# Optimization experiments

Measured on AMD Instinct MI355X. Metric: run time of the kernel, lower is better.

Reference implementation:

```python
import jax, jax.numpy as jnp
import numpy as np

B, N, F_IN, F_OUT = 1024, 16, 1024, 4096  # n_nodes=16 and n_heads=1 are structurally fixed by the module


def setup_inputs() -> dict:
    key = jax.random.key(0)
    ks = jax.random.split(key, 7)
    s1 = 1.0 / np.sqrt(F_IN)
    s2 = 1.0 / np.sqrt(F_IN * 16)
    return {
        "x": jax.random.normal(ks[0], (B, N, F_IN), jnp.float32),
        "matrix": jax.random.uniform(ks[1], (B, N, N), jnp.float32),
        "W1": jax.random.uniform(ks[2], (F_IN, F_IN), jnp.float32, -s1, s1),
        "b1": jax.random.uniform(ks[3], (F_IN,), jnp.float32, -s1, s1),
        "W_mlp": jax.random.uniform(ks[4], (F_OUT, F_IN * 16), jnp.float32, -s2, s2),
        "b_mlp": jax.random.uniform(ks[5], (F_OUT,), jnp.float32, -s2, s2),
        "a_param": jnp.float32(5.0),
    }


def _l2norm(v):
    # matches F.normalize(p=2, dim=-1, eps=1e-12)
    n = jnp.maximum(jnp.linalg.norm(v, axis=-1, keepdims=True), 1e-12)
    return v / n


def _forward(x, matrix, W1, b1, W_mlp, b_mlp, a_param):
    Bc, n, f = x.shape  # n_heads = 1, n_hidden = f
    wg = x @ W1.T + b1                                    # [B,n,f]
    gs = _l2norm(x)                                       # g_reshaped (H=1)
    gt = _l2norm(wg)                                      # g_transposed
    e = jnp.einsum('bik,bjk->bij', gs, gt)[..., None]     # [B,n,n,1] cosine scores
    eye = jnp.eye(n, dtype=x.dtype)[None, :, :, None]
    e = e * (1.0 + eye * a_param)                         # boost diagonal
    a_scores = e                                          # pre-softmax scores (used below)
    esm = jax.nn.softmax(e, axis=1)                       # softmax over dim=1
    m = matrix[..., None]                                 # [B,n,n,1]
    # MPUGAT message passing
    from_i = jnp.einsum('bitp,btkp->bikp', esm, m)        # [B,n,n,1]
    diag = jnp.einsum('bkkp->bkp', m)                     # diagonal of matrix
    from_j = esm * diag[:, None, :, :]                    # '...jkp,...kkp->...jkp'
    e2 = jnp.einsum('bikp,bjkp->bijp', from_i, from_j)    # [B,n,n,1]
    e2 = 0.5 * (e2 + jnp.transpose(e2, (0, 2, 1, 3)))
    # attention readout with PRE-softmax scores a_scores
    g = x.reshape(Bc, n, 1, f)                            # [B,n,H=1,f]
    attn = jnp.tanh(jnp.einsum('bjhf,bjih->bihf', g, a_scores))  # [B,n,1,f]
    out = attn.reshape(Bc, -1) @ W_mlp.T + b_mlp          # [B,F_OUT]
    out = jnp.broadcast_to(out[:, None, :], (Bc, 16, out.shape[-1]))  # repeat(1,16,1)
    return out, e2, m


def reference(x, matrix, W1, b1, W_mlp, b_mlp, a_param):
    return _forward(x, matrix, W1, b1, W_mlp, b_mlp, a_param)
```

## Files before the change

### kernel.cpp

```cpp
#include <hip/hip_runtime.h>
#include <math.h>

typedef short short8 __attribute__((ext_vector_type(8)));
typedef float f32x4 __attribute__((ext_vector_type(4)));
typedef unsigned short us4 __attribute__((ext_vector_type(4)));
typedef unsigned int u32x4 __attribute__((ext_vector_type(4)));
typedef unsigned short u16;
typedef unsigned int u32;

#define GAS __attribute__((address_space(1)))
#define LAS __attribute__((address_space(3)))

static __device__ __forceinline__ u16 f2bf(float f) {
    union { float f; u32 u; } v; v.f = f;
    u32 r = v.u + 0x7FFFu + ((v.u >> 16) & 1u);
    return (u16)(r >> 16);
}

static __device__ __forceinline__ u32 pk2(float a, float b) {
    return (u32)f2bf(a) | ((u32)f2bf(b) << 16);
}

static __device__ __forceinline__ u32 cvtpk(float lo, float hi) {
    u32 r;
    asm("v_cvt_pk_bf16_f32 %0, %1, %2" : "=v"(r) : "v"(lo), "v"(hi));
    return r;
}

static __device__ __forceinline__ float bf2f(u16 h) {
    union { u32 u; float f; } v; v.u = ((u32)h) << 16;
    return v.f;
}

static __device__ __forceinline__ void gll16(const void* g, void* l) {
    __builtin_amdgcn_global_load_lds((const GAS void*)g, (LAS void*)l, 16, 0, 0);
}

__global__ __launch_bounds__(256) void k_cvt_x(const float* __restrict__ x,
                                               u16* __restrict__ xb,
                                               float* __restrict__ xinv) {
    const int row = blockIdx.x, t = threadIdx.x;
    const f32x4 v = *(const f32x4*)(x + (size_t)row * 1024 + 4 * t);
    u32* dst = (u32*)(xb + (size_t)row * 1024 + 4 * t);
    dst[0] = pk2(v.x, v.y); dst[1] = pk2(v.z, v.w);
    float s = v.x * v.x + v.y * v.y + v.z * v.z + v.w * v.w;
#pragma unroll
    for (int off = 1; off < 64; off <<= 1) s += __shfl_xor(s, off, 64);
    __shared__ float red[4];
    if ((t & 63) == 0) red[t >> 6] = s;
    __syncthreads();
    if (t == 0)
        xinv[row] = 1.0f / fmaxf(sqrtf(red[0] + red[1] + red[2] + red[3]), 1e-12f);
}

__global__ __launch_bounds__(256) void k_cvt(const float* __restrict__ in,
                                             u16* __restrict__ out) {
    const size_t i = (size_t)blockIdx.x * 256 + threadIdx.x;
    const f32x4 v = *(const f32x4*)(in + 4 * i);
    u32* dst = (u32*)(out + 4 * i);
    dst[0] = pk2(v.x, v.y); dst[1] = pk2(v.z, v.w);
}

#define MFMA16(a, b, c) __builtin_amdgcn_mfma_f32_16x16x32_bf16(a, b, c, 0, 0, 0)
#define SBAR() __builtin_amdgcn_s_barrier()
#define LGKM0() do { asm volatile("s_waitcnt lgkmcnt(0)" ::: "memory"); __builtin_amdgcn_sched_barrier(0); } while (0)
#define SCHED0() __builtin_amdgcn_sched_barrier(0)
#define VMW4 asm volatile("s_waitcnt vmcnt(4)" ::: "memory")
#define VMW2 asm volatile("s_waitcnt vmcnt(2)" ::: "memory")
#define VMW0 asm volatile("s_waitcnt vmcnt(0)" ::: "memory")
#define VMW8L asm volatile("s_waitcnt vmcnt(8) lgkmcnt(0)" ::: "memory")
#define VMW0L asm volatile("s_waitcnt vmcnt(0) lgkmcnt(0)" ::: "memory")
#define LGKML asm volatile("s_waitcnt lgkmcnt(0)" ::: "memory")
#define VMNOP do {} while (0)

#define DO_TILE(ISS, VMA, VMB, VMD)                                           \
  do {                                                                        \
    short8 Af[4][2], Bf0[2][2], Bf1[2][2];                                    \
    _Pragma("unroll") for (int m = 0; m < 4; ++m) {                           \
      Af[m][0] = *(const short8*)(la + rpA[m] + sw0);                         \
      Af[m][1] = *(const short8*)(la + rpA[m] + sw1);                         \
    }                                                                         \
    _Pragma("unroll") for (int n = 0; n < 2; ++n) {                           \
      Bf0[n][0] = *(const short8*)(lb + rpB[n] + sw0);                        \
      Bf0[n][1] = *(const short8*)(lb + rpB[n] + sw1);                        \
    }                                                                         \
    if (ISS) { gll16(AG + (saO00 + knx), danext + ldst);                      \
               gll16(AG + (saO01 + knx), danext + 4096 + ldst); }             \
    SBAR(); LGKM0();                                                          \
    __builtin_amdgcn_s_setprio(1);                                            \
    _Pragma("unroll") for (int m = 0; m < 4; ++m)                             \
      _Pragma("unroll") for (int n = 0; n < 2; ++n) {                         \
        acc[m][n] = MFMA16(Af[m][0], Bf0[n][0], acc[m][n]);                   \
        acc[m][n] = MFMA16(Af[m][1], Bf0[n][1], acc[m][n]);                   \
      }                                                                       \
    __builtin_amdgcn_s_setprio(0); SCHED0(); VMA; SBAR();                     \
    _Pragma("unroll") for (int n = 0; n < 2; ++n) {                           \
      Bf1[n][0] = *(const short8*)(lb + rpB[n + 2] + sw0);                    \
      Bf1[n][1] = *(const short8*)(lb + rpB[n + 2] + sw1);                    \
    }                                                                         \
    if (ISS) { gll16(BG + (sbO00 + knx), dbnext + ldst);                      \
               gll16(BG + (sbO01 + knx), dbnext + 4096 + ldst); }             \
    SBAR(); LGKM0();                                                          \
    __builtin_amdgcn_s_setprio(1);                                            \
    _Pragma("unroll") for (int m = 0; m < 4; ++m)                             \
      _Pragma("unroll") for (int n = 0; n < 2; ++n) {                         \
        acc[m][n + 2] = MFMA16(Af[m][0], Bf1[n][0], acc[m][n + 2]);           \
        acc[m][n + 2] = MFMA16(Af[m][1], Bf1[n][1], acc[m][n + 2]);           \
      }                                                                       \
    __builtin_amdgcn_s_setprio(0); SCHED0(); VMB; SBAR();                     \
    _Pragma("unroll") for (int m = 0; m < 4; ++m) {                           \
      Af[m][0] = *(const short8*)(la + rpA[m + 4] + sw0);                     \
      Af[m][1] = *(const short8*)(la + rpA[m + 4] + sw1);                     \
    }                                                                         \
    if (ISS) { gll16(BG + (sbO10 + knx), dbnext + 8192 + ldst);               \
               gll16(BG + (sbO11 + knx), dbnext + 8192 + 4096 + ldst); }      \
    SBAR(); LGKM0();                                                          \
    __builtin_amdgcn_s_setprio(1);                                            \
    _Pragma("unroll") for (int m = 0; m < 4; ++m)                             \
      _Pragma("unroll") for (int n = 0; n < 2; ++n) {                         \
        acc[m + 4][n] = MFMA16(Af[m][0], Bf0[n][0], acc[m + 4][n]);           \
        acc[m + 4][n] = MFMA16(Af[m][1], Bf0[n][1], acc[m + 4][n]);           \
      }                                                                       \
    __builtin_amdgcn_s_setprio(0); SCHED0(); SBAR();                          \
    if (ISS) { gll16(AG + (saO10 + knx), danext + 8192 + ldst);               \
               gll16(AG + (saO11 + knx), danext + 8192 + 4096 + ldst); }      \
    __builtin_amdgcn_s_setprio(1);                                            \
    _Pragma("unroll") for (int m = 0; m < 4; ++m)                             \
      _Pragma("unroll") for (int n = 0; n < 2; ++n) {                         \
        acc[m + 4][n + 2] = MFMA16(Af[m][1], Bf1[n][1], acc[m + 4][n + 2]);   \
        acc[m + 4][n + 2] = MFMA16(Af[m][0], Bf1[n][0], acc[m + 4][n + 2]);   \
      }                                                                       \
    __builtin_amdgcn_s_setprio(0); SCHED0(); VMD; SBAR();                     \
  } while (0)

#define GT2S(ISS, KNXA, KNXB, WAITX)                                          \
  do {                                                                        \
    short8 Af[4][2], Bf0[2][2], Bf1[2][2];                                    \
    _Pragma("unroll") for (int m = 0; m < 4; ++m) {                           \
      Af[m][0] = *(const short8*)(la + rpA[m] + sw0);                         \
      Af[m][1] = *(const short8*)(la + rpA[m] + sw1);                         \
    }                                                                         \
    _Pragma("unroll") for (int n = 0; n < 2; ++n) {                           \
      Bf0[n][0] = *(const short8*)(lb + rpB[n] + sw0);                        \
      Bf0[n][1] = *(const short8*)(lb + rpB[n] + sw1);                        \
    }                                                                         \
    if (ISS) { gll16(AG + (saO00 + (KNXA)), danext + ldst);                   \
               gll16(AG + (saO01 + (KNXA)), danext + 4096 + ldst); }          \
    SBAR(); LGKM0();                                                          \
    __builtin_amdgcn_s_setprio(1);                                            \
    _Pragma("unroll") for (int k = 0; k < 2; ++k)                             \
      _Pragma("unroll") for (int m = 0; m < 4; ++m)                           \
        _Pragma("unroll") for (int n = 0; n < 2; ++n)                         \
          acc[m][n] = MFMA16(Af[m][k], Bf0[n][k], acc[m][n]);                 \
    __builtin_amdgcn_s_setprio(0); SCHED0(); SBAR();                          \
    _Pragma("unroll") for (int n = 0; n < 2; ++n) {                           \
      Bf1[n][0] = *(const short8*)(lb + rpB[n + 2] + sw0);                    \
      Bf1[n][1] = *(const short8*)(lb + rpB[n + 2] + sw1);                    \
    }                                                                         \
    if (ISS) { gll16(AG + (saO10 + (KNXA)), danext + 8192 + ldst);            \
               gll16(AG + (saO11 + (KNXA)), danext + 8192 + 4096 + ldst); }   \
    SBAR(); LGKM0();                                                          \
    __builtin_amdgcn_s_setprio(1);                                            \
    _Pragma("unroll") for (int k = 0; k < 2; ++k)                             \
      _Pragma("unroll") for (int m = 0; m < 4; ++m)                           \
        _Pragma("unroll") for (int n = 0; n < 2; ++n)                         \
          acc[m][n + 2] = MFMA16(Af[m][k], Bf1[n][k], acc[m][n + 2]);         \
    __builtin_amdgcn_s_setprio(0); SCHED0(); SBAR();                          \
    _Pragma("unroll") for (int m = 0; m < 4; ++m) {                           \
      Af[m][0] = *(const short8*)(la + rpA[m + 4] + sw0);                     \
      Af[m][1] = *(const short8*)(la + rpA[m + 4] + sw1);                     \
    }                                                                         \
    SBAR(); LGKM0();                                                          \
    __builtin_amdgcn_s_setprio(1);                                            \
    _Pragma("unroll") for (int k = 0; k < 2; ++k)                             \
      _Pragma("unroll") for (int m = 0; m < 4; ++m)                           \
        _Pragma("unroll") for (int n = 0; n < 2; ++n)                         \
          acc[m + 4][n] = MFMA16(Af[m][k], Bf0[n][k], acc[m + 4][n]);         \
    __builtin_amdgcn_s_setprio(0); SCHED0();                                  \
    if (ISS) {                                                                \
      _Pragma("unroll") for (int c = 0; c < 2; ++c) {                         \
        u32x4 wv;                                                             \
        wv.x = cvtpk(bn[2 * c].x, bn[2 * c].y);                               \
        wv.y = cvtpk(bn[2 * c].z, bn[2 * c].w);                               \
        wv.z = cvtpk(bn[2 * c + 1].x, bn[2 * c + 1].y);                       \
        wv.w = cvtpk(bn[2 * c + 1].z, bn[2 * c + 1].w);                       \
        *(u32x4*)(dbnext + c * 4096 + (tid << 3)) = wv;                       \
        bn[2 * c]     = *(const f32x4*)(BGf + bro[c] + (KNXB) + swsrc);       \
        bn[2 * c + 1] = *(const f32x4*)(BGf + bro[c] + (KNXB) + swsrc + 4);   \
      }                                                                       \
    }                                                                         \
    SBAR();                                                                   \
    __builtin_amdgcn_s_setprio(1);                                            \
    _Pragma("unroll") for (int k = 0; k < 2; ++k)                             \
      _Pragma("unroll") for (int m = 0; m < 4; ++m)                           \
        _Pragma("unroll") for (int n = 0; n < 2; ++n)                         \
          acc[m + 4][n + 2] = MFMA16(Af[m][k], Bf1[n][k], acc[m + 4][n + 2]); \
    __builtin_amdgcn_s_setprio(0); SCHED0();                                  \
    if (ISS) {                                                                \
      _Pragma("unroll") for (int c = 2; c < 4; ++c) {                         \
        u32x4 wv;                                                             \
        wv.x = cvtpk(bn[2 * c].x, bn[2 * c].y);                               \
        wv.y = cvtpk(bn[2 * c].z, bn[2 * c].w);                               \
        wv.z = cvtpk(bn[2 * c + 1].x, bn[2 * c + 1].y);                       \
        wv.w = cvtpk(bn[2 * c + 1].z, bn[2 * c + 1].w);                       \
        *(u32x4*)(dbnext + c * 4096 + (tid << 3)) = wv;                       \
        bn[2 * c]     = *(const f32x4*)(BGf + bro[c] + (KNXB) + swsrc);       \
        bn[2 * c + 1] = *(const f32x4*)(BGf + bro[c] + (KNXB) + swsrc + 4);   \
      }                                                                       \
    }                                                                         \
    WAITX; SBAR();                                                            \
  } while (0)

__global__ __launch_bounds__(512, 2) void k_gemm1_8ph(const u16* __restrict__ AG,
                                                      const u16* __restrict__ BG,
                                                      const float* __restrict__ bias,
                                                      u16* __restrict__ C,
                                                      float* __restrict__ wgn2) {
    __shared__ __align__(16) u16 LsA[2][16384];
    __shared__ __align__(16) u16 LsB[2][16384];
    const int K = 1024, NT = 16;
    const int lin = blockIdx.x;
    const int w = (lin & 7) * 32 + (lin >> 3);
    const int n0 = (w & 3) * 256;
    const int m0 = (w >> 2) * 256;

    const int tid = threadIdx.x, wave = tid >> 6, lane = tid & 63;
    const int lr = lane & 15, kq = lane >> 4;
    const int wr = wave >> 2, wc = wave & 3;

    const int trow = tid >> 3;
    const u32 swsrc = (u32)(((tid & 7) ^ (trow & 7)) * 8);
    const u32 saO00 = (u32)(m0 + 0 + trow) * (u32)K + swsrc;
    const u32 saO01 = (u32)(m0 + 128 + trow) * (u32)K + swsrc;
    const u32 saO10 = (u32)(m0 + 64 + trow) * (u32)K + swsrc;
    const u32 saO11 = (u32)(m0 + 192 + trow) * (u32)K + swsrc;
    const int q0 = trow, q1 = 64 + trow;
    const u32 sbO00 = (u32)(n0 + (q0 >> 5) * 64 + (q0 & 31)) * (u32)K + swsrc;
    const u32 sbO01 = (u32)(n0 + (q1 >> 5) * 64 + (q1 & 31)) * (u32)K + swsrc;
    const u32 sbO10 = (u32)(n0 + (q0 >> 5) * 64 + 32 + (q0 & 31)) * (u32)K + swsrc;
    const u32 sbO11 = (u32)(n0 + (q1 >> 5) * 64 + 32 + (q1 & 31)) * (u32)K + swsrc;
    const u32 ldst = (u32)wave * 512;

    int rpA[8], rpB[4];
#pragma unroll
    for (int mf = 0; mf < 8; ++mf)
        rpA[mf] = ((mf >> 2) * 128 + wr * 64 + (mf & 3) * 16 + lr) << 6;
#pragma unroll
    for (int nf = 0; nf < 4; ++nf)
        rpB[nf] = ((nf >> 1) * 128 + wc * 32 + (nf & 1) * 16 + lr) << 6;
    const int sw0 = ((0 + kq) ^ (lr & 7)) * 8;
    const int sw1 = ((4 + kq) ^ (lr & 7)) * 8;

    f32x4 acc[8][4] = {};

    gll16(AG + saO00, &LsA[0][0] + ldst);
    gll16(AG + saO01, &LsA[0][0] + 4096 + ldst);
    gll16(BG + sbO00, &LsB[0][0] + ldst);
    gll16(BG + sbO01, &LsB[0][0] + 4096 + ldst);
    gll16(BG + sbO10, &LsB[0][0] + 8192 + ldst);
    gll16(BG + sbO11, &LsB[0][0] + 8192 + 4096 + ldst);
    gll16(AG + saO10, &LsA[0][0] + 8192 + ldst);
    gll16(AG + saO11, &LsA[0][0] + 8192 + 4096 + ldst);
    VMW4;
    SBAR();

    int cur = 0;
    u32 ko = 64;
    for (int T = 0; T < NT - 1; ++T) {
        const u16* la = &LsA[cur][0];
        const u16* lb = &LsB[cur][0];
        u16* danext = &LsA[cur ^ 1][0];
        u16* dbnext = &LsB[cur ^ 1][0];
        const u32 knx = ko;
        DO_TILE(1, VMW4, VMW4, VMW4);
        cur ^= 1;
        ko += 64;
    }
    {
        const u16* la = &LsA[cur][0];
        const u16* lb = &LsB[cur][0];
        u16* danext = &LsA[cur ^ 1][0];
        u16* dbnext = &LsB[cur ^ 1][0];
        const u32 knx = 0;
        (void)danext; (void)dbnext;
        DO_TILE(0, VMW2, VMW0, VMNOP);
    }

    const int col0 = n0 + wc * 64;
    const int row0 = m0 + wr * 128;
    float bcol[4];
#pragma unroll
    for (int nf = 0; nf < 4; ++nf) bcol[nf] = bias[col0 + nf * 16 + lr];
#pragma unroll
    for (int mf = 0; mf < 8; ++mf) {
#pragma unroll
        for (int r = 0; r < 4; ++r) {
            const int row = row0 + mf * 16 + kq * 4 + r;
            float nrm = 0.f;
#pragma unroll
            for (int nf = 0; nf < 4; ++nf) {
                float v = acc[mf][nf][r] + bcol[nf];
                C[(size_t)row * 1024 + col0 + nf * 16 + lr] = f2bf(v);
                nrm += v * v;
            }
#pragma unroll
            for (int off = 1; off < 16; off <<= 1) nrm += __shfl_xor(nrm, off, 64);
            if (lr == 0) atomicAdd(&wgn2[row], nrm);
        }
    }
}

__global__ __launch_bounds__(512, 2) void k_gemm2_8ph(const u16* __restrict__ AG,
                                                      const float* __restrict__ BGf,
                                                      u16* __restrict__ part) {
    __shared__ __align__(16) u16 LsA[2][16384];
    __shared__ __align__(16) u16 LsB[2][16384];
    const int K = 16384, NT = 64;
    const int lin = blockIdx.x;
    const int w = (lin & 7) * 32 + (lin >> 3);
    const int m0 = (w & 3) * 256;
    const int z = (w >> 2) & 3;
    const int n0 = (w >> 4) * 256;
    const int kbeg = z * 4096;

    const int tid = threadIdx.x, wave = tid >> 6, lane = tid & 63;
    const int lr = lane & 15, kq = lane >> 4;
    const int wr = wave >> 2, wc = wave & 3;

    const int trow = tid >> 3;
    const u32 swsrc = (u32)(((tid & 7) ^ (trow & 7)) * 8);
    const u32 saO00 = (u32)(m0 + 0 + trow) * (u32)K + (u32)kbeg + swsrc;
    const u32 saO01 = (u32)(m0 + 128 + trow) * (u32)K + (u32)kbeg + swsrc;
    const u32 saO10 = (u32)(m0 + 64 + trow) * (u32)K + (u32)kbeg + swsrc;
    const u32 saO11 = (u32)(m0 + 192 + trow) * (u32)K + (u32)kbeg + swsrc;
    const int q0 = trow, q1 = 64 + trow;
    u32 bro[4];
    bro[0] = (u32)(n0 + (q0 >> 5) * 64 + (q0 & 31)) * 16384u + (u32)kbeg;
    bro[1] = (u32)(n0 + (q1 >> 5) * 64 + (q1 & 31)) * 16384u + (u32)kbeg;
    bro[2] = bro[0] + 32u * 16384u;
    bro[3] = bro[1] + 32u * 16384u;
    const u32 ldst = (u32)wave * 512;

    int rpA[8], rpB[4];
#pragma unroll
    for (int mf = 0; mf < 8; ++mf)
        rpA[mf] = ((mf >> 2) * 128 + wr * 64 + (mf & 3) * 16 + lr) << 6;
#pragma unroll
    for (int nf = 0; nf < 4; ++nf)
        rpB[nf] = ((nf >> 1) * 128 + wc * 32 + (nf & 1) * 16 + lr) << 6;
    const int sw0 = ((0 + kq) ^ (lr & 7)) * 8;
    const int sw1 = ((4 + kq) ^ (lr & 7)) * 8;

    f32x4 acc[8][4] = {};
    f32x4 bn[8];

    {
#pragma unroll
        for (int c = 0; c < 4; ++c) {
            bn[2 * c]     = *(const f32x4*)(BGf + bro[c] + swsrc);
            bn[2 * c + 1] = *(const f32x4*)(BGf + bro[c] + swsrc + 4);
        }
        gll16(AG + saO00, &LsA[0][0] + ldst);
        gll16(AG + saO01, &LsA[0][0] + 4096 + ldst);
        gll16(AG + saO10, &LsA[0][0] + 8192 + ldst);
        gll16(AG + saO11, &LsA[0][0] + 8192 + 4096 + ldst);
#pragma unroll
        for (int c = 0; c < 4; ++c) {
            u32x4 wv;
            wv.x = cvtpk(bn[2 * c].x, bn[2 * c].y);
            wv.y = cvtpk(bn[2 * c].z, bn[2 * c].w);
            wv.z = cvtpk(bn[2 * c + 1].x, bn[2 * c + 1].y);
            wv.w = cvtpk(bn[2 * c + 1].z, bn[2 * c + 1].w);
            *(u32x4*)(&LsB[0][0] + c * 4096 + (tid << 3)) = wv;
        }
        asm volatile("s_waitcnt vmcnt(0) lgkmcnt(0)" ::: "memory");
#pragma unroll
        for (int c = 0; c < 4; ++c) {
            bn[2 * c]     = *(const f32x4*)(BGf + bro[c] + 64 + swsrc);
            bn[2 * c + 1] = *(const f32x4*)(BGf + bro[c] + 64 + swsrc + 4);
        }
        SBAR();
    }

    int cur = 0;
    for (int T = 0; T < NT - 1; ++T) {
        const u16* la = &LsA[cur][0];
        const u16* lb = &LsB[cur][0];
        u16* danext = &LsA[cur ^ 1][0];
        u16* dbnext = &LsB[cur ^ 1][0];
        const u32 knxa = (u32)(T + 1) * 64;
        const u32 knxb = (T + 2 < NT) ? (u32)(T + 2) * 64 : 0u;
        GT2S(1, knxa, knxb, VMW8L);
        cur ^= 1;
    }
    {
        const u16* la = &LsA[cur][0];
        const u16* lb = &LsB[cur][0];
        u16* danext = &LsA[cur ^ 1][0];
        u16* dbnext = &LsB[cur ^ 1][0];
        (void)danext; (void)dbnext;
        GT2S(0, 0u, 0u, LGKML);
    }

    u16* po = part + (size_t)z * 4194304ull;
    const int col0 = n0 + wc * 64;
    const int row0 = m0 + wr * 128;
#pragma unroll
    for (int mf = 0; mf < 8; ++mf)
#pragma unroll
        for (int r = 0; r < 4; ++r) {
            const int row = row0 + mf * 16 + kq * 4 + r;
#pragma unroll
            for (int nf = 0; nf < 4; ++nf)
                po[(size_t)row * 4096 + col0 + nf * 16 + lr] = f2bf(acc[mf][nf][r]);
        }
}

__global__ __launch_bounds__(256) void k_batch_attn(const u16* xb,
                                                    const u16* __restrict__ wgb,
                                                    const float* __restrict__ xinv,
                                                    const float* __restrict__ wgn2,
                                                    const float* __restrict__ matrix,
                                                    const float* __restrict__ a_param,
                                                    float* __restrict__ e2_out,
                                                    float* __restrict__ m_out,
                                                    u16* attn_bf) {
    const int b = blockIdx.x, tid = threadIdx.x;
    const int wave = tid >> 6, lane = tid & 63;
    const int j = lane & 15, ig = (lane >> 4) * 4;

    __shared__ float qred[4][64][4];
    __shared__ float esm_l[16 * 17];
    __shared__ float fi_l[16 * 17];
    __shared__ float e2_l[16 * 17];
    __shared__ float m_l[256];
    __shared__ float as_l[256];
    __shared__ float xsh[16][256];

    {
        const size_t roff = (size_t)(b * 16 + j) * 1024 + (lane >> 4) * 8 + wave * 256;
        f32x4 acc0 = {}, acc1 = {};
#pragma unroll
        for (int kt = 0; kt < 256; kt += 64) {
            short8 xa0 = *(const short8*)(xb + roff + kt);
            short8 wa0 = *(const short8*)(wgb + roff + kt);
            short8 xa1 = *(const short8*)(xb + roff + kt + 32);
            short8 wa1 = *(const short8*)(wgb + roff + kt + 32);
            acc0 = __builtin_amdgcn_mfma_f32_16x16x32_bf16(xa0, wa0, acc0, 0, 0, 0);
            acc1 = __builtin_amdgcn_mfma_f32_16x16x32_bf16(xa1, wa1, acc1, 0, 0, 0);
        }
#pragma unroll
        for (int r = 0; r < 4; ++r) qred[wave][lane][r] = acc0[r] + acc1[r];
    }
    __syncthreads();

    if (tid < 64) {
        const int l = tid;
        const float inw = 1.0f / fmaxf(sqrtf(wgn2[b * 16 + j]), 1e-12f);
        const float boost = 1.0f + a_param[0];
        float e[4];
#pragma unroll
        for (int r = 0; r < 4; ++r) {
            const int i = ig + r;
            float v = (qred[0][l][r] + qred[1][l][r] + qred[2][l][r] + qred[3][l][r]) *
                      xinv[b * 16 + i] * inw;
            if (i == j) v *= boost;
            e[r] = v;
            as_l[i * 16 + j] = v;
        }
        float mx = fmaxf(fmaxf(e[0], e[1]), fmaxf(e[2], e[3]));
        mx = fmaxf(mx, __shfl_xor(mx, 16, 64));
        mx = fmaxf(mx, __shfl_xor(mx, 32, 64));
        float p[4], s = 0.f;
#pragma unroll
        for (int r = 0; r < 4; ++r) { p[r] = __expf(e[r] - mx); s += p[r]; }
        s += __shfl_xor(s, 16, 64);
        s += __shfl_xor(s, 32, 64);
        const float invs = 1.0f / s;
#pragma unroll
        for (int r = 0; r < 4; ++r) esm_l[(ig + r) * 17 + j] = p[r] * invs;
        const f32x4 mv = *(const f32x4*)(matrix + (size_t)b * 256 + 4 * l);
        *(f32x4*)(m_l + 4 * l) = mv;
        *(f32x4*)(m_out + (size_t)b * 256 + 4 * l) = mv;
    }
    __syncthreads();
    if (tid < 64) {
        float fi[4] = {0, 0, 0, 0};
#pragma unroll
        for (int t = 0; t < 16; ++t) {
            const float mk = m_l[t * 16 + j];
#pragma unroll
            for (int r = 0; r < 4; ++r) fi[r] += esm_l[(ig + r) * 17 + t] * mk;
        }
#pragma unroll
        for (int r = 0; r < 4; ++r) fi_l[(ig + r) * 17 + j] = fi[r];
    }
    __syncthreads();
    if (tid < 64) {
        float e2v[4] = {0, 0, 0, 0};
#pragma unroll
        for (int kk = 0; kk < 16; ++kk) {
            const float wgt = esm_l[j * 17 + kk] * m_l[kk * 16 + kk];
#pragma unroll
            for (int r = 0; r < 4; ++r) e2v[r] += fi_l[(ig + r) * 17 + kk] * wgt;
        }
#pragma unroll
        for (int r = 0; r < 4; ++r) e2_l[(ig + r) * 17 + j] = e2v[r];
    }
    __syncthreads();
    if (tid < 64) {
#pragma unroll
        for (int r = 0; r < 4; ++r) {
            const int i = ig + r;
            e2_out[(size_t)b * 256 + i * 16 + j] =
                0.5f * (e2_l[i * 17 + j] + e2_l[j * 17 + i]);
        }
    }

    for (int ch = 0; ch < 4; ++ch) {
        __syncthreads();
#pragma unroll
        for (int jj = 0; jj < 16; ++jj)
            xsh[jj][tid] = bf2f(xb[((size_t)b * 16 + jj) * 1024 + ch * 256 + tid]);
        __syncthreads();
        float accv[16] = {};
#pragma unroll
        for (int jj = 0; jj < 16; ++jj) {
            const float xv = xsh[jj][tid];
#pragma unroll
            for (int i = 0; i < 16; ++i) accv[i] = fmaf(as_l[jj * 16 + i], xv, accv[i]);
        }
#pragma unroll
        for (int i = 0; i < 16; ++i)
            attn_bf[((size_t)b * 16 + i) * 1024 + ch * 256 + tid] = f2bf(tanhf(accv[i]));
    }
}

__global__ __launch_bounds__(256) void k_bcast(const u16* __restrict__ p,
                                               const float* __restrict__ bias,
                                               float* __restrict__ out) {
    const size_t i = (size_t)blockIdx.x * 256 + threadIdx.x;
    const int o4 = (int)(i & 1023);
    const int b = (int)(i >> 14);
    const size_t src = (size_t)b * 4096 + (size_t)o4 * 4;
    f32x4 r = *(const f32x4*)(bias + (size_t)o4 * 4);
#pragma unroll
    for (int z = 0; z < 4; ++z) {
        us4 v = *(const us4*)(p + (size_t)z * 4194304ull + src);
        r.x += bf2f(v.x); r.y += bf2f(v.y); r.z += bf2f(v.z); r.w += bf2f(v.w);
    }
    *(f32x4*)(out + i * 4) = r;
}

extern "C" void kernel_launch(void* const* d_in, const int* in_sizes, int n_in,
                              void* d_out, int out_size, void* d_ws, size_t ws_size,
                              hipStream_t stream) {
    const float* x      = (const float*)d_in[0];
    const float* matrix = (const float*)d_in[1];
    const float* W1     = (const float*)d_in[2];
    const float* b1     = (const float*)d_in[3];
    const float* W_mlp  = (const float*)d_in[4];
    const float* b_mlp  = (const float*)d_in[5];
    const float* a_par  = (const float*)d_in[6];
    float* out = (float*)d_out;

    char* ws = (char*)d_ws;
    size_t off = 0;
    auto alloc = [&](size_t bytes) {
        char* p = ws + off;
        off += (bytes + 255) & ~(size_t)255;
        return p;
    };
    u16*   x_bf  = (u16*)alloc(16384ull * 1024 * 2);
    u16*   wg_bf = (u16*)alloc(16384ull * 1024 * 2);
    u16*   w1_bf = (u16*)alloc(1024ull * 1024 * 2);
    float* xinv  = (float*)alloc(16384ull * 4);
    float* wgn2  = (float*)alloc(16384ull * 4);
    u16*   attn_bf = x_bf;
    u16*   part    = wg_bf;
    float* e2_out = out + 67108864ull;
    float* m_out  = out + 67371008ull;

    hipMemsetAsync(wgn2, 0, 16384 * 4, stream);
    k_cvt_x<<<16384, 256, 0, stream>>>(x, x_bf, xinv);
    k_cvt<<<1024, 256, 0, stream>>>(W1, w1_bf);
    k_gemm1_8ph<<<256, 512, 0, stream>>>(x_bf, w1_bf, b1, wg_bf, wgn2);
    k_batch_attn<<<1024, 256, 0, stream>>>(x_bf, wg_bf, xinv, wgn2, matrix, a_par,
                                           e2_out, m_out, attn_bf);
    k_gemm2_8ph<<<256, 512, 0, stream>>>(attn_bf, W_mlp, part);
    k_bcast<<<65536, 256, 0, stream>>>(part, b_mlp, out);
}
```

Before: 370.1 us.

## Fuse W1 conversion into x conversion, reorder MFMAs, vectorize staging, fast tanh

Folds the W1 bf16 conversion into the x conversion kernel through extra blocks, removing one launch. Reorders the MFMA loops in the GEMM tile macro to iterate k outermost and drops two barriers. In the attention kernel, x is now staged in LDS as bf16 using 16-byte vector loads instead of scalar loads converted to float. tanhf is replaced with an exp-based formula. The barrier removal risks races, and the fast tanh changes rounding slightly.

Measured after the change: 339.3 us. 8.3% less time.

```diff
diff --git a/kernel.cpp b/kernel.cpp
--- a/kernel.cpp
+++ b/kernel.cpp
@@ -32,14 +32,30 @@
     return v.f;
 }
 
+static __device__ __forceinline__ float ftanh(float v) {
+    float t = __expf(-2.0f * fabsf(v));
+    float r = (1.0f - t) / (1.0f + t);
+    return copysignf(r, v);
+}
+
 static __device__ __forceinline__ void gll16(const void* g, void* l) {
     __builtin_amdgcn_global_load_lds((const GAS void*)g, (LAS void*)l, 16, 0, 0);
 }
 
 __global__ __launch_bounds__(256) void k_cvt_x(const float* __restrict__ x,
                                                u16* __restrict__ xb,
-                                               float* __restrict__ xinv) {
-    const int row = blockIdx.x, t = threadIdx.x;
+                                               float* __restrict__ xinv,
+                                               const float* __restrict__ W1,
+                                               u16* __restrict__ w1b) {
+    const int bid = blockIdx.x, t = threadIdx.x;
+    if (bid >= 16384) {
+        const size_t i = (size_t)(bid - 16384) * 256 + t;
+        const f32x4 v = *(const f32x4*)(W1 + 4 * i);
+        u32* dst = (u32*)(w1b + 4 * i);
+        dst[0] = pk2(v.x, v.y); dst[1] = pk2(v.z, v.w);
+        return;
+    }
+    const int row = bid;
     const f32x4 v = *(const f32x4*)(x + (size_t)row * 1024 + 4 * t);
     u32* dst = (u32*)(xb + (size_t)row * 1024 + 4 * t);
     dst[0] = pk2(v.x, v.y); dst[1] = pk2(v.z, v.w);
@@ -51,14 +67,6 @@
     __syncthreads();
     if (t == 0)
         xinv[row] = 1.0f / fmaxf(sqrtf(red[0] + red[1] + red[2] + red[3]), 1e-12f);
-}
-
-__global__ __launch_bounds__(256) void k_cvt(const float* __restrict__ in,
-                                             u16* __restrict__ out) {
-    const size_t i = (size_t)blockIdx.x * 256 + threadIdx.x;
-    const f32x4 v = *(const f32x4*)(in + 4 * i);
-    u32* dst = (u32*)(out + 4 * i);
-    dst[0] = pk2(v.x, v.y); dst[1] = pk2(v.z, v.w);
 }
 
 #define MFMA16(a, b, c) __builtin_amdgcn_mfma_f32_16x16x32_bf16(a, b, c, 0, 0, 0)
@@ -69,7 +77,6 @@
 #define VMW2 asm volatile("s_waitcnt vmcnt(2)" ::: "memory")
 #define VMW0 asm volatile("s_waitcnt vmcnt(0)" ::: "memory")
 #define VMW8L asm volatile("s_waitcnt vmcnt(8) lgkmcnt(0)" ::: "memory")
-#define VMW0L asm volatile("s_waitcnt vmcnt(0) lgkmcnt(0)" ::: "memory")
 #define LGKML asm volatile("s_waitcnt lgkmcnt(0)" ::: "memory")
 #define VMNOP do {} while (0)
 
@@ -88,11 +95,10 @@
                gll16(AG + (saO01 + knx), danext + 4096 + ldst); }             \
     SBAR(); LGKM0();                                                          \
     __builtin_amdgcn_s_setprio(1);                                            \
-    _Pragma("unroll") for (int m = 0; m < 4; ++m)                             \
-      _Pragma("unroll") for (int n = 0; n < 2; ++n) {                         \
-        acc[m][n] = MFMA16(Af[m][0], Bf0[n][0], acc[m][n]);                   \
-        acc[m][n] = MFMA16(Af[m][1], Bf0[n][1], acc[m][n]);                   \
-      }                                                                       \
+    _Pragma("unroll") for (int k = 0; k < 2; ++k)                             \
+      _Pragma("unroll") for (int m = 0; m < 4; ++m)                           \
+        _Pragma("unroll") for (int n = 0; n < 2; ++n)                         \
+          acc[m][n] = MFMA16(Af[m][k], Bf0[n][k], acc[m][n]);                 \
     __builtin_amdgcn_s_setprio(0); SCHED0(); VMA; SBAR();                     \
     _Pragma("unroll") for (int n = 0; n < 2; ++n) {                           \
       Bf1[n][0] = *(const short8*)(lb + rpB[n + 2] + sw0);                    \
@@ -102,11 +108,10 @@
                gll16(BG + (sbO01 + knx), dbnext + 4096 + ldst); }             \
     SBAR(); LGKM0();                                                          \
     __builtin_amdgcn_s_setprio(1);                                            \
-    _Pragma("unroll") for (int m = 0; m < 4; ++m)                             \
-      _Pragma("unroll") for (int n = 0; n < 2; ++n) {                         \
-        acc[m][n + 2] = MFMA16(Af[m][0], Bf1[n][0], acc[m][n + 2]);           \
-        acc[m][n + 2] = MFMA16(Af[m][1], Bf1[n][1], acc[m][n + 2]);           \
-      }                                                                       \
+    _Pragma("unroll") for (int k = 0; k < 2; ++k)                             \
+      _Pragma("unroll") for (int m = 0; m < 4; ++m)                           \
+        _Pragma("unroll") for (int n = 0; n < 2; ++n)                         \
+          acc[m][n + 2] = MFMA16(Af[m][k], Bf1[n][k], acc[m][n + 2]);         \
     __builtin_amdgcn_s_setprio(0); SCHED0(); VMB; SBAR();                     \
     _Pragma("unroll") for (int m = 0; m < 4; ++m) {                           \
       Af[m][0] = *(const short8*)(la + rpA[m + 4] + sw0);                     \
@@ -116,20 +121,18 @@
                gll16(BG + (sbO11 + knx), dbnext + 8192 + 4096 + ldst); }      \
     SBAR(); LGKM0();                                                          \
     __builtin_amdgcn_s_setprio(1);                                            \
-    _Pragma("unroll") for (int m = 0; m < 4; ++m)                             \
-      _Pragma("unroll") for (int n = 0; n < 2; ++n) {                         \
-        acc[m + 4][n] = MFMA16(Af[m][0], Bf0[n][0], acc[m + 4][n]);           \
-        acc[m + 4][n] = MFMA16(Af[m][1], Bf0[n][1], acc[m + 4][n]);           \
-      }                                                                       \
-    __builtin_amdgcn_s_setprio(0); SCHED0(); SBAR();                          \
+    _Pragma("unroll") for (int k = 0; k < 2; ++k)                             \
+      _Pragma("unroll") for (int m = 0; m < 4; ++m)                           \
+        _Pragma("unroll") for (int n = 0; n < 2; ++n)                         \
+          acc[m + 4][n] = MFMA16(Af[m][k], Bf0[n][k], acc[m + 4][n]);         \
+    __builtin_amdgcn_s_setprio(0); SCHED0();                                  \
     if (ISS) { gll16(AG + (saO10 + knx), danext + 8192 + ldst);               \
                gll16(AG + (saO11 + knx), danext + 8192 + 4096 + ldst); }      \
     __builtin_amdgcn_s_setprio(1);                                            \
-    _Pragma("unroll") for (int m = 0; m < 4; ++m)                             \
-      _Pragma("unroll") for (int n = 0; n < 2; ++n) {                         \
-        acc[m + 4][n + 2] = MFMA16(Af[m][1], Bf1[n][1], acc[m + 4][n + 2]);   \
-        acc[m + 4][n + 2] = MFMA16(Af[m][0], Bf1[n][0], acc[m + 4][n + 2]);   \
-      }                                                                       \
+    _Pragma("unroll") for (int k = 0; k < 2; ++k)                             \
+      _Pragma("unroll") for (int m = 0; m < 4; ++m)                           \
+        _Pragma("unroll") for (int n = 0; n < 2; ++n)                         \
+          acc[m + 4][n + 2] = MFMA16(Af[m][k], Bf1[n][k], acc[m + 4][n + 2]); \
     __builtin_amdgcn_s_setprio(0); SCHED0(); VMD; SBAR();                     \
   } while (0)
 
@@ -189,7 +192,6 @@
         bn[2 * c + 1] = *(const f32x4*)(BGf + bro[c] + (KNXB) + swsrc + 4);   \
       }                                                                       \
     }                                                                         \
-    SBAR();                                                                   \
     __builtin_amdgcn_s_setprio(1);                                            \
     _Pragma("unroll") for (int k = 0; k < 2; ++k)                             \
       _Pragma("unroll") for (int m = 0; m < 4; ++m)                           \
@@ -435,7 +437,7 @@
     __shared__ float e2_l[16 * 17];
     __shared__ float m_l[256];
     __shared__ float as_l[256];
-    __shared__ float xsh[16][256];
+    __shared__ u16 xsh[16][256];
 
     {
         const size_t roff = (size_t)(b * 16 + j) * 1024 + (lane >> 4) * 8 + wave * 256;
@@ -517,22 +519,24 @@
         }
     }
 
+    const int srow = tid >> 4;
+    const int scol = (tid & 15) * 16;
     for (int ch = 0; ch < 4; ++ch) {
         __syncthreads();
-#pragma unroll
-        for (int jj = 0; jj < 16; ++jj)
-            xsh[jj][tid] = bf2f(xb[((size_t)b * 16 + jj) * 1024 + ch * 256 + tid]);
+        const u16* src = xb + ((size_t)b * 16 + srow) * 1024 + ch * 256 + scol;
+        *(short8*)&xsh[srow][scol] = *(const short8*)src;
+        *(short8*)&xsh[srow][scol + 8] = *(const short8*)(src + 8);
         __syncthreads();
         float accv[16] = {};
 #pragma unroll
         for (int jj = 0; jj < 16; ++jj) {
-            const float xv = xsh[jj][tid];
+            const float xv = bf2f(xsh[jj][tid]);
 #pragma unroll
             for (int i = 0; i < 16; ++i) accv[i] = fmaf(as_l[jj * 16 + i], xv, accv[i]);
         }
 #pragma unroll
         for (int i = 0; i < 16; ++i)
-            attn_bf[((size_t)b * 16 + i) * 1024 + ch * 256 + tid] = f2bf(tanhf(accv[i]));
+            attn_bf[((size_t)b * 16 + i) * 1024 + ch * 256 + tid] = f2bf(ftanh(accv[i]));
     }
 }
 
@@ -582,8 +586,7 @@
     float* m_out  = out + 67371008ull;
 
     hipMemsetAsync(wgn2, 0, 16384 * 4, stream);
-    k_cvt_x<<<16384, 256, 0, stream>>>(x, x_bf, xinv);
-    k_cvt<<<1024, 256, 0, stream>>>(W1, w1_bf);
+    k_cvt_x<<<17408, 256, 0, stream>>>(x, x_bf, xinv, W1, w1_bf);
     k_gemm1_8ph<<<256, 512, 0, stream>>>(x_bf, w1_bf, b1, wg_bf, wgn2);
     k_batch_attn<<<1024, 256, 0, stream>>>(x_bf, wg_bf, xinv, wgn2, matrix, a_par,
                                            e2_out, m_out, attn_bf);
```
